# Kernel optimization log

Hardware: AMD Instinct MI355X
Metric: run time of the kernel (lower is better)

## Reference

```python
import jax, jax.numpy as jnp
import numpy as np

B, S, D, NH, DFF, NL, C = 16, 1024, 768, 4, 3072, 2, 3


def _w(k, shape, s=0.02):
    return jax.random.normal(k, shape, dtype=jnp.float32) * s


def setup_inputs() -> dict:
    key = jax.random.key(0)
    ks = iter(jax.random.split(key, 40))
    inp = {}
    inp['spans_embedding'] = jax.random.normal(next(ks), (B, S, D), dtype=jnp.float32)
    lengths = jax.random.randint(next(ks), (B,), S // 2, S + 1)
    inp['span_mask'] = (jnp.arange(S)[None, :] < lengths[:, None]).astype(jnp.int32)
    inp['mha_in_w'] = _w(next(ks), (3 * D, D)); inp['mha_in_b'] = jnp.zeros((3 * D,), jnp.float32)
    inp['mha_out_w'] = _w(next(ks), (D, D)); inp['mha_out_b'] = jnp.zeros((D,), jnp.float32)
    inp['asp_mlp_w'] = _w(next(ks), (D, D)); inp['asp_mlp_b'] = jnp.zeros((D,), jnp.float32)
    inp['opi_mlp_w'] = _w(next(ks), (D, D)); inp['opi_mlp_b'] = jnp.zeros((D,), jnp.float32)
    inp['imp_asp_cls_w'] = _w(next(ks), (2, D)); inp['imp_asp_cls_b'] = jnp.zeros((2,), jnp.float32)
    inp['imp_opi_cls_w'] = _w(next(ks), (2, D)); inp['imp_opi_cls_b'] = jnp.zeros((2,), jnp.float32)
    for pre in ('fwd', 'rev'):
        inp[pre + '_inter_w'] = _w(next(ks), (NL, DFF, D)); inp[pre + '_inter_b'] = jnp.zeros((NL, DFF), jnp.float32)
        inp[pre + '_out_w'] = _w(next(ks), (NL, D, DFF)); inp[pre + '_out_b'] = jnp.zeros((NL, D), jnp.float32)
        inp[pre + '_ln_g'] = jnp.ones((NL, D), jnp.float32); inp[pre + '_ln_b'] = jnp.zeros((NL, D), jnp.float32)
    inp['cls_asp_w'] = _w(next(ks), (C, D)); inp['cls_asp_b'] = jnp.zeros((C,), jnp.float32)
    inp['cls_opi_w'] = _w(next(ks), (C, D)); inp['cls_opi_b'] = jnp.zeros((C,), jnp.float32)
    return inp


def _layer_norm(x, g, b, eps=1e-12):
    m = jnp.mean(x, axis=-1, keepdims=True)
    v = jnp.mean(jnp.square(x - m), axis=-1, keepdims=True)
    return (x - m) * jax.lax.rsqrt(v + eps) * g + b


def _decoder_stack(h, Wi, bi, Wo, bo, g, b):
    # Step_1_module: BERT Intermediate (gelu) + Output (residual + LayerNorm); dropout is eval-mode identity.
    def step(h, p):
        Wi_, bi_, Wo_, bo_, g_, b_ = p
        inter = jax.nn.gelu(jnp.einsum('bsd,fd->bsf', h, Wi_) + bi_, approximate=False)
        out = jnp.einsum('bsf,df->bsd', inter, Wo_) + bo_
        return _layer_norm(out + h, g_, b_), None
    h, _ = jax.lax.scan(step, h, (Wi, bi, Wo, bo, g, b))
    return h


def _forward(spans_embedding, span_mask, mha_in_w, mha_in_b, mha_out_w, mha_out_b,
             asp_mlp_w, asp_mlp_b, opi_mlp_w, opi_mlp_b,
             imp_asp_cls_w, imp_asp_cls_b, imp_opi_cls_w, imp_opi_cls_b,
             fwd_inter_w, fwd_inter_b, fwd_out_w, fwd_out_b, fwd_ln_g, fwd_ln_b,
             rev_inter_w, rev_inter_b, rev_out_w, rev_out_b, rev_ln_g, rev_ln_b,
             cls_asp_w, cls_asp_b, cls_opi_w, cls_opi_b):
    x = spans_embedding  # [B, S, D]
    Bq, Sq, Dq = x.shape
    hd = Dq // NH
    # nn.MultiheadAttention(D, 4) self-attention with key_padding_mask = ~span_mask
    qkv = x @ mha_in_w.T + mha_in_b  # [B, S, 3D]
    q, k, v = jnp.split(qkv, 3, axis=-1)
    def heads(t):
        return t.reshape(Bq, Sq, NH, hd).transpose(0, 2, 1, 3)  # [B, H, S, hd]
    scores = jnp.einsum('bhqd,bhkd->bhqk', heads(q), heads(k)) / jnp.sqrt(jnp.float32(hd))
    key_pad = (span_mask == 0)[:, None, None, :]
    scores = jnp.where(key_pad, jnp.float32(-1e30), scores)
    ctx = jnp.einsum('bhqk,bhkd->bhqd', jax.nn.softmax(scores, axis=-1), heads(v))
    ctx = ctx.transpose(0, 2, 1, 3).reshape(Bq, Sq, Dq)
    embedding = (ctx @ mha_out_w.T + mha_out_b).mean(axis=1)  # mean over span dim -> [B, D]
    e1 = embedding @ asp_mlp_w.T + asp_mlp_b
    e2 = embedding @ opi_mlp_w.T + opi_mlp_b
    imp_asp = e1 @ imp_asp_cls_w.T + imp_asp_cls_b  # [B, 2] (dropout eval = identity)
    imp_opi = e2 @ imp_opi_cls_w.T + imp_opi_cls_b
    # per-sample scatter: [i,0]=e1 then [i,idx]=e2 (se1); [i,idx]=e2 then [i,0]=e1 (se2)
    idx = jnp.sum(span_mask, axis=-1) - 1
    bidx = jnp.arange(Bq)
    se1 = x.at[:, 0].set(e1).at[bidx, idx].set(e2)
    se2 = x.at[bidx, idx].set(e2).at[:, 0].set(e1)
    se1 = _decoder_stack(se1, fwd_inter_w, fwd_inter_b, fwd_out_w, fwd_out_b, fwd_ln_g, fwd_ln_b)
    se2 = _decoder_stack(se2, rev_inter_w, rev_inter_b, rev_out_w, rev_out_b, rev_ln_g, rev_ln_b)
    logits_asp = se1 @ cls_asp_w.T + cls_asp_b  # [B, S, C]
    logits_opi = se2 @ cls_opi_w.T + cls_opi_b
    return (logits_asp, logits_opi, x, se1, se2, imp_asp, imp_opi, e1, e2)


def reference(spans_embedding, span_mask, mha_in_w, mha_in_b, mha_out_w, mha_out_b,
              asp_mlp_w, asp_mlp_b, opi_mlp_w, opi_mlp_b,
              imp_asp_cls_w, imp_asp_cls_b, imp_opi_cls_w, imp_opi_cls_b,
              fwd_inter_w, fwd_inter_b, fwd_out_w, fwd_out_b, fwd_ln_g, fwd_ln_b,
              rev_inter_w, rev_inter_b, rev_out_w, rev_out_b, rev_ln_g, rev_ln_b,
              cls_asp_w, cls_asp_b, cls_opi_w, cls_opi_b):
    return _forward(spans_embedding, span_mask, mha_in_w, mha_in_b, mha_out_w, mha_out_b,
                    asp_mlp_w, asp_mlp_b, opi_mlp_w, opi_mlp_b,
                    imp_asp_cls_w, imp_asp_cls_b, imp_opi_cls_w, imp_opi_cls_b,
                    fwd_inter_w, fwd_inter_b, fwd_out_w, fwd_out_b, fwd_ln_g, fwd_ln_b,
                    rev_inter_w, rev_inter_b, rev_out_w, rev_out_b, rev_ln_g, rev_ln_b,
                    cls_asp_w, cls_asp_b, cls_opi_w, cls_opi_b)
```

## Files before the change

kernel.cpp:

```cpp
#include <hip/hip_runtime.h>
#include <hip/hip_bf16.h>
#include <stdint.h>

#define Bb 16
#define Ss 1024
#define Dd 768
#define HDd 192

typedef __attribute__((ext_vector_type(8))) short short8;
typedef __attribute__((ext_vector_type(4))) short short4a;
typedef __attribute__((ext_vector_type(4))) float f32x4;

__device__ __forceinline__ short f2bf(float f) {
  union { __hip_bfloat16 h; short s; } u;
  u.h = __float2bfloat16(f);
  return u.s;
}
__device__ __forceinline__ short8 cvt8(float4 lo, float4 hi) {
  short8 r;
  r[0] = f2bf(lo.x); r[1] = f2bf(lo.y); r[2] = f2bf(lo.z); r[3] = f2bf(lo.w);
  r[4] = f2bf(hi.x); r[5] = f2bf(hi.y); r[6] = f2bf(hi.z); r[7] = f2bf(hi.w);
  return r;
}
__device__ __forceinline__ void gload_lds16(const void* g, void* l) {
  __builtin_amdgcn_global_load_lds(
      (const __attribute__((address_space(1))) void*)g,
      (__attribute__((address_space(3))) void*)l, 16, 0, 0);
}

enum { EPI_F32 = 0, EPI_GELU = 1, EPI_MEANACC = 2, EPI_RESAT = 3 };

template <int EPI, int OBF>
__global__ __launch_bounds__(256) void gemm_bf(
    const short* __restrict__ A, const short* __restrict__ Bw,
    const float* __restrict__ bias, void* __restrict__ outp,
    const int N, const int K)
{
  constexpr int TM = 128, TN = 128, BK = 64;
  __shared__ __align__(16) short As[TM * BK];
  __shared__ __align__(16) short Bs[TN * BK];

  const int tid = threadIdx.x;
  const int wave = tid >> 6, lane = tid & 63;
  const int l16 = lane & 15, quad = lane >> 4;
  const int wm = wave >> 1, wn = wave & 1;
  const size_t m0 = (size_t)blockIdx.y * TM;
  const size_t n0 = (size_t)blockIdx.x * TN;
  const int kz = blockIdx.z;
  const int kbeg = (EPI == EPI_RESAT) ? kz * (K >> 2) : 0;
  const int kend = (EPI == EPI_RESAT) ? kbeg + (K >> 2) : K;

  const int srow = tid >> 3;
  const int sunit = (tid & 7) ^ (srow & 7);
  const short* Ag = A + (m0 + srow) * K + sunit * 8;
  const short* Bg = Bw + (n0 + srow) * K + sunit * 8;
  short* Asd = &As[tid * 8];
  short* Bsd = &Bs[tid * 8];

  f32x4 acc[4][4];
#pragma unroll
  for (int i = 0; i < 4; ++i)
#pragma unroll
    for (int j = 0; j < 4; ++j) acc[i][j] = (f32x4){0.f, 0.f, 0.f, 0.f};

#pragma unroll 1
  for (int k0 = kbeg; k0 < kend; k0 += BK) {
    __syncthreads();
#pragma unroll
    for (int i = 0; i < 4; ++i) {
      gload_lds16(Ag + (size_t)(32 * i) * K + k0, Asd + 2048 * i);
      gload_lds16(Bg + (size_t)(32 * i) * K + k0, Bsd + 2048 * i);
    }
    __syncthreads();

#pragma unroll
    for (int kh = 0; kh < 2; ++kh) {
      short8 af[4], bfr[4];
#pragma unroll
      for (int i = 0; i < 4; ++i) {
        const int arow = wm * 64 + i * 16 + l16;
        const int pu = ((kh * 4 + quad) ^ (l16 & 7)) * 8;
        af[i]  = *(const short8*)&As[arow * BK + pu];
        bfr[i] = *(const short8*)&Bs[(wn * 64 + i * 16 + l16) * BK + pu];
      }
#pragma unroll
      for (int mt = 0; mt < 4; ++mt)
#pragma unroll
        for (int nt = 0; nt < 4; ++nt)
          acc[mt][nt] = __builtin_amdgcn_mfma_f32_16x16x32_bf16(af[mt], bfr[nt], acc[mt][nt], 0, 0, 0);
    }
  }

  if constexpr (EPI == EPI_MEANACC) {
    float* eacc = (float*)outp;
    const int b = (int)(m0 >> 10);
#pragma unroll
    for (int nt = 0; nt < 4; ++nt) {
      float cs = 0.f;
#pragma unroll
      for (int mt = 0; mt < 4; ++mt)
#pragma unroll
        for (int r = 0; r < 4; ++r) cs += acc[mt][nt][r];
      cs += __shfl_xor(cs, 16, 64);
      cs += __shfl_xor(cs, 32, 64);
      if (quad == 0) {
        const int col = (int)n0 + wn * 64 + nt * 16 + l16;
        atomicAdd(&eacc[b * Dd + col], cs);
      }
    }
  } else if constexpr (EPI == EPI_RESAT) {
    float* outf = (float*)outp;
#pragma unroll
    for (int nt = 0; nt < 4; ++nt) {
      const size_t col = n0 + wn * 64 + nt * 16 + l16;
      const float bv = (kz == 0) ? bias[col] : 0.f;
#pragma unroll
      for (int mt = 0; mt < 4; ++mt) {
#pragma unroll
        for (int r = 0; r < 4; ++r) {
          const size_t row = m0 + wm * 64 + mt * 16 + quad * 4 + r;
          atomicAdd(&outf[row * N + col], acc[mt][nt][r] + bv);
        }
      }
    }
  } else {
#pragma unroll
    for (int nt = 0; nt < 4; ++nt) {
      const size_t col = n0 + wn * 64 + nt * 16 + l16;
      const float bv = bias[col];
#pragma unroll
      for (int mt = 0; mt < 4; ++mt) {
#pragma unroll
        for (int r = 0; r < 4; ++r) {
          const size_t row = m0 + wm * 64 + mt * 16 + quad * 4 + r;
          float v = acc[mt][nt][r] + bv;
          if constexpr (EPI == EPI_GELU)
            v = 0.5f * v * (1.f + erff(v * 0.70710678118654752f));
          if constexpr (OBF)
            ((short*)outp)[row * N + col] = f2bf(v);
          else
            ((float*)outp)[row * N + col] = v;
        }
      }
    }
  }
}

__global__ __launch_bounds__(256, 2) void flash_attn(
    const short* __restrict__ qkv, const int* __restrict__ idxp,
    short* __restrict__ ctx)
{
  __shared__ __align__(16) short Ks[64 * 192];
  __shared__ __align__(16) short Vt[192 * 64];
  __shared__ __align__(16) short Ps[4][16 * 64];

  const int tid = threadIdx.x, wave = tid >> 6, lane = tid & 63;
  const int l16 = lane & 15, quad = lane >> 4;
  const int qt = blockIdx.x, h = blockIdx.y, b = blockIdx.z;
  const int L = idxp[b] + 1;
  const short* base = qkv + (size_t)b * Ss * (3 * Dd);
  const short* Kb = base + Dd + h * HDd;
  const short* Vb = base + 2 * Dd + h * HDd;

  short8 qf[6];
  {
    const short* qp = base + (size_t)(qt * 64 + wave * 16 + l16) * (3 * Dd) + h * HDd;
#pragma unroll
    for (int c = 0; c < 6; ++c) qf[c] = *(const short8*)(qp + c * 32 + quad * 8);
  }

  f32x4 acc[12];
#pragma unroll
  for (int i = 0; i < 12; ++i) acc[i] = (f32x4){0.f, 0.f, 0.f, 0.f};
  float m = -3.0e38f, l = 0.f;
  const float scale = 0.07216878364870322f;

#pragma unroll 1
  for (int kt = 0; kt < 16; ++kt) {
    const int k0 = kt * 64;
    if (k0 >= L) break;
    __syncthreads();

#pragma unroll
    for (int i = 0; i < 6; ++i) {
      const int c = tid + 256 * i;
      const int kk = c / 24, u = c % 24;
      gload_lds16(Kb + (size_t)(k0 + kk) * (3 * Dd) + (u ^ (kk & 7)) * 8, &Ks[c * 8]);
    }
#pragma unroll
    for (int i = 0; i < 6; ++i) {
      const int c = tid + 256 * i;
      const int kp2 = (c & 31) * 2, dc = (c >> 5) * 4;
      const short* vp = Vb + (size_t)(k0 + kp2) * (3 * Dd) + dc;
      const short4a va  = *(const short4a*)vp;
      const short4a vb4 = *(const short4a*)(vp + 3 * Dd);
#pragma unroll
      for (int j = 0; j < 4; ++j) {
        const int d = dc + j;
        const unsigned int pr = (unsigned int)(unsigned short)va[j] |
                                ((unsigned int)(unsigned short)vb4[j] << 16);
        *(unsigned int*)&Vt[(d * 64 + kp2) ^ ((d & 7) << 3)] = pr;
      }
    }
    __syncthreads();

    f32x4 accS[4];
#pragma unroll
    for (int mt = 0; mt < 4; ++mt) accS[mt] = (f32x4){0.f, 0.f, 0.f, 0.f};
#pragma unroll
    for (int c = 0; c < 6; ++c) {
      short8 kf[4];
#pragma unroll
      for (int mt = 0; mt < 4; ++mt) {
        const int row = mt * 16 + l16;
        kf[mt] = *(const short8*)&Ks[(row * 192 + c * 32 + quad * 8) ^ ((l16 & 7) << 3)];
      }
#pragma unroll
      for (int mt = 0; mt < 4; ++mt)
        accS[mt] = __builtin_amdgcn_mfma_f32_16x16x32_bf16(kf[mt], qf[c], accS[mt], 0, 0, 0);
    }

    float tm = -3.0e38f;
#pragma unroll
    for (int mt = 0; mt < 4; ++mt) {
      const int kg = k0 + mt * 16 + quad * 4;
#pragma unroll
      for (int r = 0; r < 4; ++r) {
        const float sv = (kg + r < L) ? accS[mt][r] * scale : -1.0e30f;
        accS[mt][r] = sv;
        tm = fmaxf(tm, sv);
      }
    }
    tm = fmaxf(tm, __shfl_xor(tm, 16));
    tm = fmaxf(tm, __shfl_xor(tm, 32));
    const float mn = fmaxf(m, tm);
    const bool stay = (mn == m);
    const float sf = __expf(m - mn);
    m = mn;
    l *= sf;

    float rs = 0.f;
#pragma unroll
    for (int mt = 0; mt < 4; ++mt) {
      short4a pw;
#pragma unroll
      for (int r = 0; r < 4; ++r) {
        const float p = __expf(accS[mt][r] - mn);
        rs += p;
        pw[r] = f2bf(p);
      }
      *(short4a*)&Ps[wave][(l16 * 64 + mt * 16 + quad * 4) ^ ((l16 & 7) << 3)] = pw;
    }
    rs += __shfl_xor(rs, 16);
    rs += __shfl_xor(rs, 32);
    l += rs;

    if (!__all(stay)) {
      f32x4 sv_;
#pragma unroll
      for (int r = 0; r < 4; ++r) sv_[r] = __shfl(sf, quad * 4 + r);
#pragma unroll
      for (int nt = 0; nt < 12; ++nt)
#pragma unroll
        for (int r = 0; r < 4; ++r) acc[nt][r] *= sv_[r];
    }

#pragma unroll
    for (int ks = 0; ks < 2; ++ks) {
      const short8 pa =
          *(const short8*)&Ps[wave][(l16 * 64 + ks * 32 + quad * 8) ^ ((l16 & 7) << 3)];
#pragma unroll
      for (int nt = 0; nt < 12; ++nt) {
        const int d = nt * 16 + l16;
        const short8 vb =
            *(const short8*)&Vt[(d * 64 + ks * 32 + quad * 8) ^ ((d & 7) << 3)];
        acc[nt] = __builtin_amdgcn_mfma_f32_16x16x32_bf16(pa, vb, acc[nt], 0, 0, 0);
      }
    }
  }

  const float inv = 1.f / l;
  f32x4 iv;
#pragma unroll
  for (int r = 0; r < 4; ++r) iv[r] = __shfl(inv, quad * 4 + r);
  const int qrow = qt * 64 + wave * 16;
#pragma unroll
  for (int r = 0; r < 4; ++r) {
    short* cp = ctx + ((size_t)b * Ss + qrow + quad * 4 + r) * Dd + h * HDd + l16;
#pragma unroll
    for (int nt = 0; nt < 12; ++nt) cp[nt * 16] = f2bf(acc[nt][r] * iv[r]);
  }
}

__global__ __launch_bounds__(256) void calc_idx(const int* __restrict__ mask, int* __restrict__ idx) {
  __shared__ int sm[256];
  const int b = blockIdx.x, tid = threadIdx.x;
  int s = 0;
  for (int i = tid; i < Ss; i += 256) s += mask[b * Ss + i];
  sm[tid] = s;
  __syncthreads();
  for (int o = 128; o > 0; o >>= 1) {
    if (tid < o) sm[tid] += sm[tid + o];
    __syncthreads();
  }
  if (tid == 0) idx[b] = sm[0] - 1;
}

__global__ __launch_bounds__(256) void cvt_bf(const float* __restrict__ s,
                                              short* __restrict__ d, int n8) {
  const int i = blockIdx.x * 256 + threadIdx.x;
  if (i < n8)
    *(short8*)(d + (size_t)i * 8) = cvt8(((const float4*)s)[i * 2],
                                         ((const float4*)s)[i * 2 + 1]);
}

__global__ __launch_bounds__(256) void e12_kernel(
    const float* __restrict__ eacc, const float* __restrict__ outb,
    const float* __restrict__ aw, const float* __restrict__ ab,
    const float* __restrict__ ow, const float* __restrict__ ob,
    float* __restrict__ e1, float* __restrict__ e2)
{
  const int id = blockIdx.x * 256 + threadIdx.x;
  const int which = (id >= 12288);
  const int r = which ? id - 12288 : id;
  const int n = r >> 4, b = r & 15;
  const float* w = (which ? ow : aw) + (size_t)n * Dd;
  const float* ea = eacc + b * Dd;
  float s = 0.f;
#pragma unroll 4
  for (int d = 0; d < Dd; d += 4) {
    const float4 wv = *(const float4*)(w + d);
    const float4 ev = *(const float4*)(ea + d);
    const float4 bv = *(const float4*)(outb + d);
    s += (ev.x * (1.f / 1024.f) + bv.x) * wv.x + (ev.y * (1.f / 1024.f) + bv.y) * wv.y
       + (ev.z * (1.f / 1024.f) + bv.z) * wv.z + (ev.w * (1.f / 1024.f) + bv.w) * wv.w;
  }
  s += which ? ob[n] : ab[n];
  (which ? e2 : e1)[b * Dd + n] = s;
}

__global__ __launch_bounds__(64) void imp_kernel(
    const float* __restrict__ e1, const float* __restrict__ e2,
    const float* __restrict__ wa, const float* __restrict__ ba,
    const float* __restrict__ wo, const float* __restrict__ bo,
    float* __restrict__ outa, float* __restrict__ outo)
{
  const int id = blockIdx.x, lane = threadIdx.x;
  const int b = id >> 2, which = (id >> 1) & 1, c = id & 1;
  const float* e = which ? e2 : e1;
  const float* w = which ? wo : wa;
  const float* bb = which ? bo : ba;
  float s = 0.f;
  for (int d = lane; d < Dd; d += 64) s += e[b * Dd + d] * w[c * Dd + d];
  for (int off = 32; off > 0; off >>= 1) s += __shfl_xor(s, off, 64);
  if (lane == 0) {
    float* o = which ? outo : outa;
    o[b * 2 + c] = s + bb[c];
  }
}

__global__ __launch_bounds__(256) void scatter_kernel(
    const float* __restrict__ x, const float* __restrict__ e1,
    const float* __restrict__ e2, const int* __restrict__ idx,
    float* __restrict__ h1, float* __restrict__ h2)
{
  const int row = blockIdx.x;
  const int b = row >> 10, s = row & 1023;
  const int ix = idx[b];
  const size_t base = (size_t)row * Dd;
  for (int i = threadIdx.x; i < Dd; i += 256) {
    const float xv = x[base + i];
    const float v1 = e1[b * Dd + i];
    const float v2 = e2[b * Dd + i];
    h1[base + i] = (s == ix) ? v2 : ((s == 0) ? v1 : xv);
    h2[base + i] = (s == 0) ? v1 : ((s == ix) ? v2 : xv);
  }
}

__global__ __launch_bounds__(64) void ln_kernel(
    float* __restrict__ h, short* __restrict__ hb,
    const float* __restrict__ g, const float* __restrict__ bb)
{
  const int row = blockIdx.x, lane = threadIdx.x;
  const size_t base = (size_t)row * Dd;
  float v[12];
  float s = 0.f, sq = 0.f;
#pragma unroll
  for (int t = 0; t < 12; ++t) {
    const int i = t * 64 + lane;
    const float val = h[base + i];
    v[t] = val;
    s += val;
    sq += val * val;
  }
#pragma unroll
  for (int off = 32; off > 0; off >>= 1) {
    s += __shfl_xor(s, off, 64);
    sq += __shfl_xor(sq, off, 64);
  }
  const float m = s * (1.f / 768.f);
  float var = sq * (1.f / 768.f) - m * m;
  var = fmaxf(var, 0.f);
  const float r = rsqrtf(var + 1e-12f);
#pragma unroll
  for (int t = 0; t < 12; ++t) {
    const int i = t * 64 + lane;
    const float o = (v[t] - m) * r * g[i] + bb[i];
    h[base + i] = o;
    hb[base + i] = f2bf(o);
  }
}

__global__ __launch_bounds__(64) void logits_kernel(
    const float* __restrict__ h1, const float* __restrict__ h2,
    const float* __restrict__ wa, const float* __restrict__ ba,
    const float* __restrict__ wo, const float* __restrict__ bo,
    float* __restrict__ outa, float* __restrict__ outo)
{
  const int id = blockIdx.x, lane = threadIdx.x;
  const int which = id >> 14;
  const int row = id & 16383;
  const float* h = which ? h2 : h1;
  const float* w = which ? wo : wa;
  const float* bc = which ? bo : ba;
  const size_t base = (size_t)row * Dd;
  float s0 = 0.f, s1 = 0.f, s2 = 0.f;
#pragma unroll
  for (int t = 0; t < 12; ++t) {
    const int i = t * 64 + lane;
    const float hv = h[base + i];
    s0 += hv * w[i];
    s1 += hv * w[Dd + i];
    s2 += hv * w[2 * Dd + i];
  }
#pragma unroll
  for (int off = 32; off > 0; off >>= 1) {
    s0 += __shfl_xor(s0, off, 64);
    s1 += __shfl_xor(s1, off, 64);
    s2 += __shfl_xor(s2, off, 64);
  }
  if (lane == 0) {
    float* o = which ? outo : outa;
    o[(size_t)row * 3 + 0] = s0 + bc[0];
    o[(size_t)row * 3 + 1] = s1 + bc[1];
    o[(size_t)row * 3 + 2] = s2 + bc[2];
  }
}

__global__ __launch_bounds__(256) void copy16(const uint4* __restrict__ s, uint4* __restrict__ d, int n) {
  const int i = blockIdx.x * 256 + threadIdx.x;
  if (i < n) d[i] = s[i];
}

extern "C" void kernel_launch(void* const* d_in, const int* in_sizes, int n_in,
                              void* d_out, int out_size, void* d_ws, size_t ws_size,
                              hipStream_t stream)
{
  (void)in_sizes; (void)n_in; (void)out_size; (void)d_ws; (void)ws_size;
  const float* x        = (const float*)d_in[0];
  const int*   mask     = (const int*)d_in[1];
  const float* mha_in_w = (const float*)d_in[2];
  const float* mha_in_b = (const float*)d_in[3];
  const float* mha_out_w= (const float*)d_in[4];
  const float* mha_out_b= (const float*)d_in[5];
  const float* asp_w    = (const float*)d_in[6];
  const float* asp_b    = (const float*)d_in[7];
  const float* opi_w    = (const float*)d_in[8];
  const float* opi_b    = (const float*)d_in[9];
  const float* ia_w     = (const float*)d_in[10];
  const float* ia_b     = (const float*)d_in[11];
  const float* io_w     = (const float*)d_in[12];
  const float* io_b     = (const float*)d_in[13];
  const float* cls_a_w  = (const float*)d_in[26];
  const float* cls_a_b  = (const float*)d_in[27];
  const float* cls_o_w  = (const float*)d_in[28];
  const float* cls_o_b  = (const float*)d_in[29];

  float* out   = (float*)d_out;
  float* o_la  = out;
  float* o_lo  = out + 49152;
  float* o_x   = out + 98304;
  float* o_se1 = o_x + 12582912;
  float* o_se2 = o_se1 + 12582912;
  float* o_ia  = o_se2 + 12582912;
  float* o_io  = o_ia + 32;
  float* o_e1  = o_io + 32;
  float* o_e2  = o_e1 + 12288;

  short* x_bf   = (short*)o_x;
  short* ctx_bf = (short*)(o_x + 6291456);
  short* qkv_bf = (short*)o_se1;
  short* win_bf = (short*)(o_se1 + 18874368);
  short* wout_bf= (short*)(o_se1 + 19759104);
  float* eacc   = o_x;
  int*   idxp   = (int*)o_lo;

  short* interbuf = (short*)o_x;
  short* hb       = (short*)(o_x + 6291456);
  short* wib      = (short*)(o_x + 7864320);
  short* wob      = (short*)(o_x + 10223616);

  float* h1 = o_se1;
  float* h2 = o_se2;

  calc_idx<<<Bb, 256, 0, stream>>>(mask, idxp);

  cvt_bf<<<6144, 256, 0, stream>>>(x, x_bf, 1572864);
  cvt_bf<<<864, 256, 0, stream>>>(mha_in_w, win_bf, 221184);
  cvt_bf<<<288, 256, 0, stream>>>(mha_out_w, wout_bf, 73728);

  gemm_bf<EPI_F32, 1><<<dim3(18, 128), 256, 0, stream>>>(
      x_bf, win_bf, mha_in_b, qkv_bf, 2304, 768);
  flash_attn<<<dim3(16, 4, 16), 256, 0, stream>>>(qkv_bf, idxp, ctx_bf);

  hipMemsetAsync(eacc, 0, Bb * Dd * sizeof(float), stream);
  gemm_bf<EPI_MEANACC, 0><<<dim3(6, 128), 256, 0, stream>>>(
      ctx_bf, wout_bf, nullptr, eacc, 768, 768);

  e12_kernel<<<96, 256, 0, stream>>>(eacc, mha_out_b, asp_w, asp_b, opi_w, opi_b,
                                     o_e1, o_e2);
  imp_kernel<<<64, 64, 0, stream>>>(o_e1, o_e2, ia_w, ia_b, io_w, io_b, o_ia, o_io);
  scatter_kernel<<<16384, 256, 0, stream>>>(x, o_e1, o_e2, idxp, h1, h2);

  for (int st = 0; st < 2; ++st) {
    float* h = st ? h2 : h1;
    const float* Wi = (const float*)d_in[14 + st * 6];
    const float* bi = (const float*)d_in[15 + st * 6];
    const float* Wo = (const float*)d_in[16 + st * 6];
    const float* bo = (const float*)d_in[17 + st * 6];
    const float* lg = (const float*)d_in[18 + st * 6];
    const float* lb = (const float*)d_in[19 + st * 6];
    cvt_bf<<<2304, 256, 0, stream>>>(Wi, wib, 589824);
    cvt_bf<<<2304, 256, 0, stream>>>(Wo, wob, 589824);
    for (int c = 0; c < 4; ++c) {
      float* hc = h + (size_t)c * 4096 * Dd;
      cvt_bf<<<1536, 256, 0, stream>>>(hc, hb, 393216);
      for (int l = 0; l < 2; ++l) {
        gemm_bf<EPI_GELU, 1><<<dim3(3072 / 128, 4096 / 128), 256, 0, stream>>>(
            hb, wib + (size_t)l * 3072 * 768, bi + l * 3072, interbuf, 3072, 768);
        gemm_bf<EPI_RESAT, 0><<<dim3(768 / 128, 4096 / 128, 4), 256, 0, stream>>>(
            interbuf, wob + (size_t)l * 768 * 3072, bo + l * 768, hc, 768, 3072);
        ln_kernel<<<4096, 64, 0, stream>>>(hc, hb, lg + l * 768, lb + l * 768);
      }
    }
  }

  logits_kernel<<<32768, 64, 0, stream>>>(h1, h2, cls_a_w, cls_a_b, cls_o_w, cls_o_b,
                                          o_la, o_lo);
  copy16<<<12288, 256, 0, stream>>>((const uint4*)x, (uint4*)o_x, 3145728);
}
```

Before: 2.254 ms.

## Use workspace for decoder buffers, process full batch, fold x copy into scatter

When the workspace is large enough, the decoder intermediate and weight buffers move from the output tensor into the workspace. The FFN then runs on all 16384 rows in one chunk instead of four, which cuts launch count and gives larger GEMM grids. The copy of x into its output slot is folded into the scatter kernel. Flash attention reuses the K tile LDS region for P, with an added barrier, so it can target 3 blocks per CU instead of 2. This costs an extra barrier per key tile, and the fast path depends on the workspace size provided.

```diff
diff --git a/kernel.cpp b/kernel.cpp
--- a/kernel.cpp
+++ b/kernel.cpp
@@ -146,13 +146,12 @@
   }
 }
 
-__global__ __launch_bounds__(256, 2) void flash_attn(
+__global__ __launch_bounds__(256, 3) void flash_attn(
     const short* __restrict__ qkv, const int* __restrict__ idxp,
     short* __restrict__ ctx)
 {
   __shared__ __align__(16) short Ks[64 * 192];
   __shared__ __align__(16) short Vt[192 * 64];
-  __shared__ __align__(16) short Ps[4][16 * 64];
 
   const int tid = threadIdx.x, wave = tid >> 6, lane = tid & 63;
   const int l16 = lane & 15, quad = lane >> 4;
@@ -161,6 +160,7 @@
   const short* base = qkv + (size_t)b * Ss * (3 * Dd);
   const short* Kb = base + Dd + h * HDd;
   const short* Vb = base + 2 * Dd + h * HDd;
+  short* Ps = &Ks[wave * 1024];
 
   short8 qf[6];
   {
@@ -239,6 +239,8 @@
     m = mn;
     l *= sf;
 
+    __syncthreads();
+
     float rs = 0.f;
 #pragma unroll
     for (int mt = 0; mt < 4; ++mt) {
@@ -249,7 +251,7 @@
         rs += p;
         pw[r] = f2bf(p);
       }
-      *(short4a*)&Ps[wave][(l16 * 64 + mt * 16 + quad * 4) ^ ((l16 & 7) << 3)] = pw;
+      *(short4a*)&Ps[(l16 * 64 + mt * 16 + quad * 4) ^ ((l16 & 7) << 3)] = pw;
     }
     rs += __shfl_xor(rs, 16);
     rs += __shfl_xor(rs, 32);
@@ -268,7 +270,7 @@
 #pragma unroll
     for (int ks = 0; ks < 2; ++ks) {
       const short8 pa =
-          *(const short8*)&Ps[wave][(l16 * 64 + ks * 32 + quad * 8) ^ ((l16 & 7) << 3)];
+          *(const short8*)&Ps[(l16 * 64 + ks * 32 + quad * 8) ^ ((l16 & 7) << 3)];
 #pragma unroll
       for (int nt = 0; nt < 12; ++nt) {
         const int d = nt * 16 + l16;
@@ -362,7 +364,7 @@
 __global__ __launch_bounds__(256) void scatter_kernel(
     const float* __restrict__ x, const float* __restrict__ e1,
     const float* __restrict__ e2, const int* __restrict__ idx,
-    float* __restrict__ h1, float* __restrict__ h2)
+    float* __restrict__ h1, float* __restrict__ h2, float* __restrict__ xc)
 {
   const int row = blockIdx.x;
   const int b = row >> 10, s = row & 1023;
@@ -374,6 +376,7 @@
     const float v2 = e2[b * Dd + i];
     h1[base + i] = (s == ix) ? v2 : ((s == 0) ? v1 : xv);
     h2[base + i] = (s == 0) ? v1 : ((s == ix) ? v2 : xv);
+    if (xc) xc[base + i] = xv;
   }
 }
 
@@ -456,7 +459,7 @@
                               void* d_out, int out_size, void* d_ws, size_t ws_size,
                               hipStream_t stream)
 {
-  (void)in_sizes; (void)n_in; (void)out_size; (void)d_ws; (void)ws_size;
+  (void)in_sizes; (void)n_in; (void)out_size;
   const float* x        = (const float*)d_in[0];
   const int*   mask     = (const int*)d_in[1];
   const float* mha_in_w = (const float*)d_in[2];
@@ -495,10 +498,14 @@
   float* eacc   = o_x;
   int*   idxp   = (int*)o_lo;
 
-  short* interbuf = (short*)o_x;
-  short* hb       = (short*)(o_x + 6291456);
-  short* wib      = (short*)(o_x + 7864320);
-  short* wob      = (short*)(o_x + 10223616);
+  const bool big = (ws_size >= (size_t)146 * 1024 * 1024);
+  short* ws_s = (short*)d_ws;
+  short* interbuf = big ? ws_s            : (short*)o_x;
+  short* hb       = big ? ws_s + 50331648 : (short*)(o_x + 6291456);
+  short* wib      = big ? ws_s + 62914560 : (short*)(o_x + 7864320);
+  short* wob      = big ? ws_s + 67633152 : (short*)(o_x + 10223616);
+  const int Mc = big ? 16384 : 4096;
+  const int nc = big ? 1 : 4;
 
   float* h1 = o_se1;
   float* h2 = o_se2;
@@ -520,7 +527,8 @@
   e12_kernel<<<96, 256, 0, stream>>>(eacc, mha_out_b, asp_w, asp_b, opi_w, opi_b,
                                      o_e1, o_e2);
   imp_kernel<<<64, 64, 0, stream>>>(o_e1, o_e2, ia_w, ia_b, io_w, io_b, o_ia, o_io);
-  scatter_kernel<<<16384, 256, 0, stream>>>(x, o_e1, o_e2, idxp, h1, h2);
+  scatter_kernel<<<16384, 256, 0, stream>>>(x, o_e1, o_e2, idxp, h1, h2,
+                                            big ? o_x : nullptr);
 
   for (int st = 0; st < 2; ++st) {
     float* h = st ? h2 : h1;
@@ -532,20 +540,21 @@
     const float* lb = (const float*)d_in[19 + st * 6];
     cvt_bf<<<2304, 256, 0, stream>>>(Wi, wib, 589824);
     cvt_bf<<<2304, 256, 0, stream>>>(Wo, wob, 589824);
-    for (int c = 0; c < 4; ++c) {
-      float* hc = h + (size_t)c * 4096 * Dd;
-      cvt_bf<<<1536, 256, 0, stream>>>(hc, hb, 393216);
+    for (int c = 0; c < nc; ++c) {
+      float* hc = h + (size_t)c * Mc * Dd;
+      cvt_bf<<<Mc * 96 / 256, 256, 0, stream>>>(hc, hb, Mc * 96);
       for (int l = 0; l < 2; ++l) {
-        gemm_bf<EPI_GELU, 1><<<dim3(3072 / 128, 4096 / 128), 256, 0, stream>>>(
+        gemm_bf<EPI_GELU, 1><<<dim3(3072 / 128, Mc / 128), 256, 0, stream>>>(
             hb, wib + (size_t)l * 3072 * 768, bi + l * 3072, interbuf, 3072, 768);
-        gemm_bf<EPI_RESAT, 0><<<dim3(768 / 128, 4096 / 128, 4), 256, 0, stream>>>(
+        gemm_bf<EPI_RESAT, 0><<<dim3(768 / 128, Mc / 128, 4), 256, 0, stream>>>(
             interbuf, wob + (size_t)l * 768 * 3072, bo + l * 768, hc, 768, 3072);
-        ln_kernel<<<4096, 64, 0, stream>>>(hc, hb, lg + l * 768, lb + l * 768);
+        ln_kernel<<<Mc, 64, 0, stream>>>(hc, hb, lg + l * 768, lb + l * 768);
       }
     }
   }
 
   logits_kernel<<<32768, 64, 0, stream>>>(h1, h2, cls_a_w, cls_a_b, cls_o_w, cls_o_b,
                                           o_la, o_lo);
-  copy16<<<12288, 256, 0, stream>>>((const uint4*)x, (uint4*)o_x, 3145728);
-}
+  if (!big)
+    copy16<<<12288, 256, 0, stream>>>((const uint4*)x, (uint4*)o_x, 3145728);
+}
```

Result: faster. 2.092 ms (-7.2%).
